# Performance work log

Measured on AMD Instinct MI355X. Metric: run time of the kernel, lower is better.

Reference implementation:

```python
import jax, jax.numpy as jnp
import numpy as np

N = 50000      # nodes
E = 800000     # edges (avg degree 16)
IN = 256       # in_channels
H = 128        # hidden_channels
LOC = 512      # location projection dim
EPS_BN = 1e-5
EPS_COS = 1e-8
NEG_SLOPE = 0.01


def setup_inputs() -> dict:
    key = jax.random.key(0)
    ks = jax.random.split(key, 16)
    s = 1.0 / np.sqrt(IN)
    sh = 1.0 / np.sqrt(H)
    return {
        "x": jax.random.normal(ks[0], (N, IN), dtype=jnp.float32),
        "edge_index": jax.random.randint(ks[1], (2, E), 0, N, dtype=jnp.int64),
        "bn_gamma": jax.random.uniform(ks[2], (IN,), dtype=jnp.float32, minval=0.5, maxval=1.5),
        "bn_beta": jax.random.normal(ks[3], (IN,), dtype=jnp.float32) * 0.1,
        "bn_mean": jax.random.normal(ks[4], (IN,), dtype=jnp.float32) * 0.1,
        "bn_var": jax.random.uniform(ks[5], (IN,), dtype=jnp.float32, minval=0.5, maxval=1.5),
        "W_lin": jax.random.uniform(ks[6], (IN, H), dtype=jnp.float32, minval=-s, maxval=s),
        "b_lin": jnp.zeros((H,), jnp.float32),
        "W1": jax.random.uniform(ks[7], (H, H), dtype=jnp.float32, minval=-sh, maxval=sh),
        "b1": jnp.zeros((H,), jnp.float32),
        "W2": jax.random.uniform(ks[8], (H, H), dtype=jnp.float32, minval=-sh, maxval=sh),
        "b2": jnp.zeros((H,), jnp.float32),
        "W_loc": jax.random.uniform(ks[9], (IN, LOC), dtype=jnp.float32, minval=-s, maxval=s),
        "b_loc": jnp.zeros((LOC,), jnp.float32),
        "loc_vec": jax.random.normal(ks[10], (N, IN), dtype=jnp.float32),
    }


def _leaky_relu(v):
    return jnp.where(v >= 0, v, NEG_SLOPE * v)


def _gcn_conv(h, W, b, src, dst, dinv, n):
    # PyG GCNConv (eval): D^{-1/2}(A+I)D^{-1/2} h W + b ; src/dst include self-loops
    hw = h @ W                                   # [n, H]
    coef = (dinv[src] * dinv[dst])[:, None]      # [e+n, 1]
    msg = hw[src] * coef                         # edge gather + scale
    return jax.ops.segment_sum(msg, dst, num_segments=n) + b


def reference(x, edge_index, bn_gamma, bn_beta, bn_mean, bn_var,
              W_lin, b_lin, W1, b1, W2, b2, W_loc, b_loc, loc_vec):
    n = x.shape[0]
    src = edge_index[0]
    dst = edge_index[1]
    loops = jnp.arange(n, dtype=src.dtype)
    # supply direction: src->dst ; demand direction: reversed edges
    s_src = jnp.concatenate([src, loops]); s_dst = jnp.concatenate([dst, loops])
    d_src = jnp.concatenate([dst, loops]); d_dst = jnp.concatenate([src, loops])

    def dinv_of(dd):
        deg = jax.ops.segment_sum(jnp.ones(dd.shape[0], x.dtype), dd, num_segments=n)
        return jnp.where(deg > 0, jax.lax.rsqrt(deg), 0.0)

    dinv_s = dinv_of(s_dst)
    dinv_d = dinv_of(d_dst)

    # BatchNorm1d (eval) + input Linear
    xb = (x - bn_mean) * jax.lax.rsqrt(bn_var + EPS_BN) * bn_gamma + bn_beta
    h = xb @ W_lin + b_lin

    # two GCN layers per direction (dropout is identity in eval)
    s1 = _leaky_relu(_gcn_conv(h, W1, b1, s_src, s_dst, dinv_s, n))
    s2 = _leaky_relu(_gcn_conv(s1, W2, b2, s_src, s_dst, dinv_s, n))
    r1 = _leaky_relu(_gcn_conv(h, W1, b1, d_src, d_dst, dinv_d, n))
    r2 = _leaky_relu(_gcn_conv(r1, W2, b2, d_src, d_dst, dinv_d, n))

    # edge-gather dot-product logits
    logits = jnp.sum(s2[src] * r2[dst], axis=1)  # [E]

    # location cosine-similarity per edge
    loc = loc_vec @ W_loc + b_loc                # [N, 512]
    l1 = loc[src]; l2 = loc[dst]
    cos = jnp.sum(l1 * l2, axis=1) / jnp.maximum(
        jnp.linalg.norm(l1, axis=1) * jnp.linalg.norm(l2, axis=1), EPS_COS)
    return logits / cos
```

## Files before the change

kernel.cpp:

```cpp
#include <hip/hip_runtime.h>

#define IN_C 256
#define H_C  128
#define LOC_C 512
#define EPS_BN 1e-5f
#define PSTR 136

typedef unsigned int u32;

__device__ __forceinline__ float lrelu(float v) { return v >= 0.0f ? v : 0.01f * v; }

__global__ void detect_i64(const int* ei, int* flag) {
  if (threadIdx.x == 0 && blockIdx.x == 0) {
    int z = 1;
    for (int i = 1; i < 128; i += 2) if (ei[i] != 0) { z = 0; break; }
    *flag = z;
  }
}

__device__ __forceinline__ int ld_edge(const int* ei, int is64, int idx) {
  return is64 ? ei[2 * idx] : ei[idx];
}

__global__ void sentinel_kernel(float* out, int n) {
  int i = blockIdx.x * blockDim.x + threadIdx.x;
  if (i < n) out[i] = 1.2345e9f;
}

__global__ void bn_prep(const float* __restrict__ g, const float* __restrict__ be,
                        const float* __restrict__ mu, const float* __restrict__ var,
                        float* __restrict__ scale, float* __restrict__ shift) {
  int c = threadIdx.x;
  float s = rsqrtf(var[c] + EPS_BN) * g[c];
  scale[c] = s;
  shift[c] = be[c] - mu[c] * s;
}

__global__ void degree_kernel(const int* __restrict__ ei, const int* __restrict__ flag,
                              int E, u32* __restrict__ deg_s, u32* __restrict__ deg_d) {
  int e = blockIdx.x * blockDim.x + threadIdx.x;
  if (e >= E) return;
  int is64 = *flag;
  int s = ld_edge(ei, is64, e);
  int d = ld_edge(ei, is64, E + e);
  atomicAdd(&deg_s[d], 1u);
  atomicAdd(&deg_d[s], 1u);
}

__global__ __launch_bounds__(1024) void scan_kernel(const u32* __restrict__ deg,
                                                    u32* __restrict__ rowptr,
                                                    u32* __restrict__ cursor,
                                                    float* __restrict__ dinv,
                                                    int N, int E) {
  __shared__ u32 part[1024];
  int dir = blockIdx.x;
  const u32* dg = deg + (size_t)dir * N;
  u32* rp = rowptr + (size_t)dir * (N + 1);
  u32* cu = cursor + (size_t)dir * N;
  float* dv = dinv + (size_t)dir * N;
  int t = threadIdx.x;
  int CH = (N + 1023) >> 10;
  int base = t * CH;
  u32 s = 0;
  for (int i = 0; i < CH; ++i) { int idx = base + i; if (idx < N) s += dg[idx]; }
  part[t] = s;
  __syncthreads();
  for (int off = 1; off < 1024; off <<= 1) {
    u32 v = (t >= off) ? part[t - off] : 0u;
    __syncthreads();
    part[t] += v;
    __syncthreads();
  }
  u32 run = (t > 0) ? part[t - 1] : 0u;
  for (int i = 0; i < CH; ++i) {
    int idx = base + i;
    if (idx < N) {
      rp[idx] = run;
      cu[idx] = run;
      u32 c = dg[idx];
      dv[idx] = rsqrtf((float)(c + 1u));
      run += c;
    }
  }
  if (t == 0) rp[N] = (u32)E;
}

__global__ void fill_kernel(const int* __restrict__ ei, const int* __restrict__ flag, int E,
                            u32* __restrict__ cur_s, u32* __restrict__ cur_d,
                            u32* __restrict__ col_s, u32* __restrict__ col_d,
                            u32* __restrict__ eid_d) {
  int e = blockIdx.x * blockDim.x + threadIdx.x;
  if (e >= E) return;
  int is64 = *flag;
  int s = ld_edge(ei, is64, e);
  int d = ld_edge(ei, is64, E + e);
  u32 ps = atomicAdd(&cur_s[d], 1u);
  col_s[ps] = (u32)s;
  u32 pd = atomicAdd(&cur_d[s], 1u);
  col_d[pd] = (u32)d;
  eid_d[pd] = (u32)e;
}

#define GM 128
#define GN 128
#define GK 16
#define ASTR (GM + 4)
#define BSTR (GN + 4)
template<bool BN_A, bool BIAS>
__global__ __launch_bounds__(256) void gemm_kernel(const float* __restrict__ A,
                                                   const float* __restrict__ B,
                                                   float* __restrict__ C,
                                                   int M, int K, int Ncols,
                                                   const float* __restrict__ bias,
                                                   const float* __restrict__ bnsc,
                                                   const float* __restrict__ bnsh) {
  __shared__ float As[GK][ASTR];
  __shared__ float Bs[GK][BSTR];
  int t = threadIdx.x;
  int tx = t & 15, ty = t >> 4;
  int m0 = blockIdx.x * GM;
  int n0 = blockIdx.y * GN;
  float acc[8][8] = {};
  for (int kk = 0; kk < K; kk += GK) {
#pragma unroll
    for (int i = 0; i < 2; ++i) {
      int idx = t * 2 + i;
      int row = idx >> 2;
      int kq = idx & 3;
      int gr = m0 + row;
      float4 v = make_float4(0.f, 0.f, 0.f, 0.f);
      if (gr < M) v = *(const float4*)(A + (size_t)gr * K + kk + kq * 4);
      if (BN_A) {
        float4 sc = *(const float4*)(bnsc + kk + kq * 4);
        float4 sh = *(const float4*)(bnsh + kk + kq * 4);
        v.x = fmaf(v.x, sc.x, sh.x); v.y = fmaf(v.y, sc.y, sh.y);
        v.z = fmaf(v.z, sc.z, sh.z); v.w = fmaf(v.w, sc.w, sh.w);
      }
      As[kq * 4 + 0][row] = v.x; As[kq * 4 + 1][row] = v.y;
      As[kq * 4 + 2][row] = v.z; As[kq * 4 + 3][row] = v.w;
    }
#pragma unroll
    for (int i = 0; i < 2; ++i) {
      int idx = t * 2 + i;
      int kr = idx >> 5;
      int cq = idx & 31;
      *(float4*)&Bs[kr][cq * 4] = *(const float4*)(B + (size_t)(kk + kr) * Ncols + n0 + cq * 4);
    }
    __syncthreads();
#pragma unroll
    for (int k = 0; k < GK; ++k) {
      float4 a0 = *(const float4*)&As[k][ty * 4];
      float4 a1 = *(const float4*)&As[k][ty * 4 + 64];
      float4 b0 = *(const float4*)&Bs[k][tx * 4];
      float4 b1 = *(const float4*)&Bs[k][tx * 4 + 64];
      float ar[8] = {a0.x, a0.y, a0.z, a0.w, a1.x, a1.y, a1.z, a1.w};
      float br[8] = {b0.x, b0.y, b0.z, b0.w, b1.x, b1.y, b1.z, b1.w};
#pragma unroll
      for (int ii = 0; ii < 8; ++ii)
#pragma unroll
        for (int jj = 0; jj < 8; ++jj)
          acc[ii][jj] = fmaf(ar[ii], br[jj], acc[ii][jj]);
    }
    __syncthreads();
  }
#pragma unroll
  for (int ii = 0; ii < 8; ++ii) {
    int gr = m0 + ((ii < 4) ? (ty * 4 + ii) : (64 + ty * 4 + ii - 4));
    if (gr < M) {
      float4 o0 = make_float4(acc[ii][0], acc[ii][1], acc[ii][2], acc[ii][3]);
      float4 o1 = make_float4(acc[ii][4], acc[ii][5], acc[ii][6], acc[ii][7]);
      if (BIAS) {
        float4 c0 = *(const float4*)(bias + n0 + tx * 4);
        float4 c1 = *(const float4*)(bias + n0 + 64 + tx * 4);
        o0.x += c0.x; o0.y += c0.y; o0.z += c0.z; o0.w += c0.w;
        o1.x += c1.x; o1.y += c1.y; o1.z += c1.z; o1.w += c1.w;
      }
      *(float4*)(C + (size_t)gr * Ncols + n0 + tx * 4) = o0;
      *(float4*)(C + (size_t)gr * Ncols + n0 + 64 + tx * 4) = o1;
    }
  }
}

__device__ __forceinline__ float4 fma4s(float4 v, float s, float4 c) {
  c.x = fmaf(v.x, s, c.x); c.y = fmaf(v.y, s, c.y);
  c.z = fmaf(v.z, s, c.z); c.w = fmaf(v.w, s, c.w);
  return c;
}

__global__ __launch_bounds__(256) void agg_kernel(const float* __restrict__ hw,
                                                  const float* __restrict__ dinv,
                                                  const u32* __restrict__ rowptr,
                                                  const u32* __restrict__ col,
                                                  const float* __restrict__ bias,
                                                  float* __restrict__ out, int N) {
  int wid = (blockIdx.x * blockDim.x + threadIdx.x) >> 6;
  int lane = threadIdx.x & 63;
  int half = lane >> 5, hl = lane & 31;
  int node = wid * 2 + half;
  if (node >= N) return;
  float di = dinv[node];
  float4 acc = *(const float4*)(hw + (size_t)node * H_C + hl * 4);
  acc.x *= di; acc.y *= di; acc.z *= di; acc.w *= di;
  u32 beg = rowptr[node], end = rowptr[node + 1];
  u32 k = beg;
  for (; k + 2 <= end; k += 2) {
    u32 j0 = col[k], j1 = col[k + 1];
    float dj0 = dinv[j0], dj1 = dinv[j1];
    float4 v0 = *(const float4*)(hw + (size_t)j0 * H_C + hl * 4);
    float4 v1 = *(const float4*)(hw + (size_t)j1 * H_C + hl * 4);
    acc = fma4s(v0, dj0, acc);
    acc = fma4s(v1, dj1, acc);
  }
  if (k < end) {
    u32 j0 = col[k];
    float dj0 = dinv[j0];
    float4 v0 = *(const float4*)(hw + (size_t)j0 * H_C + hl * 4);
    acc = fma4s(v0, dj0, acc);
  }
  float4 b4 = *(const float4*)(bias + hl * 4);
  float4 o;
  o.x = lrelu(fmaf(acc.x, di, b4.x));
  o.y = lrelu(fmaf(acc.y, di, b4.y));
  o.z = lrelu(fmaf(acc.z, di, b4.z));
  o.w = lrelu(fmaf(acc.w, di, b4.w));
  *(float4*)(out + (size_t)node * H_C + hl * 4) = o;
}

__device__ __forceinline__ float np_tree_combine(float r) {
  r = __fadd_rn(r, __shfl_xor(r, 1));
  r = __fadd_rn(r, __shfl_xor(r, 2));
  r = __fadd_rn(r, __shfl_xor(r, 4));
  r = __fadd_rn(r, __shfl_xor(r, 8));
  r = __fadd_rn(r, __shfl_xor(r, 16));
  return r;
}

__global__ __launch_bounds__(256) void norm_np_kernel(const float* __restrict__ loc,
                                                      float* __restrict__ norms, int N) {
  __shared__ float buf[4][PSTR * 4];
  int wib = threadIdx.x >> 6;
  int lane = threadIdx.x & 63;
  int u = blockIdx.x * 4 + wib;
  if (u >= N) return;
  const float* row = loc + (size_t)u * LOC_C;
#pragma unroll
  for (int i = 0; i < 2; ++i) {
    int w = lane + i * 64;
    float4 v4 = *(const float4*)(row + w * 4);
    *(float4*)&buf[wib][(w >> 5) * PSTR + ((w * 4) & 127)] = v4;
  }
  if (lane < 32) {
    int b = lane >> 3, j = lane & 7;
    const float* p = &buf[wib][b * PSTR + j];
    float v = p[0];
    float r = __fmul_rn(v, v);
#pragma unroll
    for (int t = 1; t < 16; ++t) {
      v = p[8 * t];
      r = __fadd_rn(r, __fmul_rn(v, v));
    }
    r = np_tree_combine(r);
    if (lane == 0) norms[u] = sqrtf(r);
  }
}

__global__ __launch_bounds__(256) void edge_np_kernel(const float* __restrict__ s2,
                                                      const float* __restrict__ r2,
                                                      const float* __restrict__ loc,
                                                      const float* __restrict__ norms,
                                                      const u32* __restrict__ rowptr_d,
                                                      const u32* __restrict__ col_d,
                                                      const u32* __restrict__ eid_d,
                                                      float* __restrict__ out, int N) {
  __shared__ float l1s[4][PSTR * 4];
  __shared__ float l2s[4][PSTR * 4];
  int wib = threadIdx.x >> 6;
  int lane = threadIdx.x & 63;
  int u = blockIdx.x * 4 + wib;
  if (u >= N) return;
  {
    const float* row = loc + (size_t)u * LOC_C;
#pragma unroll
    for (int i = 0; i < 2; ++i) {
      int w = lane + i * 64;
      float4 v4 = *(const float4*)(row + w * 4);
      *(float4*)&l1s[wib][(w >> 5) * PSTR + ((w * 4) & 127)] = v4;
    }
  }
  float2 su = *(const float2*)(s2 + (size_t)u * H_C + lane * 2);
  float nu = norms[u];
  int b = lane >> 3, j = lane & 7;
  u32 beg = rowptr_d[u], end = rowptr_d[u + 1];
  for (u32 k = beg; k < end; ++k) {
    u32 v = col_d[k];
    u32 e = eid_d[k];
    {
      const float* row = loc + (size_t)v * LOC_C;
#pragma unroll
      for (int i = 0; i < 2; ++i) {
        int w = lane + i * 64;
        float4 v4 = *(const float4*)(row + w * 4);
        *(float4*)&l2s[wib][(w >> 5) * PSTR + ((w * 4) & 127)] = v4;
      }
    }
    float2 rv = *(const float2*)(r2 + (size_t)v * H_C + lane * 2);
    float da = su.x * rv.x + su.y * rv.y;
#pragma unroll
    for (int off = 32; off; off >>= 1) da += __shfl_xor(da, off);
    float dt = 0.f;
    if (lane < 32) {
      const float* p1 = &l1s[wib][b * PSTR + j];
      const float* p2 = &l2s[wib][b * PSTR + j];
      float r = __fmul_rn(p1[0], p2[0]);
#pragma unroll
      for (int t = 1; t < 16; ++t)
        r = __fadd_rn(r, __fmul_rn(p1[8 * t], p2[8 * t]));
      dt = np_tree_combine(r);
    }
    if (lane == 0) {
      float n1n2 = __fmul_rn(nu, norms[v]);
      float den = fmaxf(n1n2, 1e-8f);
      float cosv = __fdiv_rn(dt, den);
      out[e] = __fdiv_rn(da, cosv);
    }
  }
}

extern "C" void kernel_launch(void* const* d_in, const int* in_sizes, int n_in,
                              void* d_out, int out_size, void* d_ws, size_t ws_size,
                              hipStream_t stream) {
  const float* x     = (const float*)d_in[0];
  const int*   ei    = (const int*)d_in[1];
  const float* bn_g  = (const float*)d_in[2];
  const float* bn_b  = (const float*)d_in[3];
  const float* bn_m  = (const float*)d_in[4];
  const float* bn_v  = (const float*)d_in[5];
  const float* W_lin = (const float*)d_in[6];
  const float* b_lin = (const float*)d_in[7];
  const float* W1    = (const float*)d_in[8];
  const float* b1    = (const float*)d_in[9];
  const float* W2    = (const float*)d_in[10];
  const float* b2    = (const float*)d_in[11];
  const float* W_loc = (const float*)d_in[12];
  const float* lv    = (const float*)d_in[14];
  float* out = (float*)d_out;

  int N = in_sizes[0] / IN_C;
  int E = in_sizes[1] / 2;

  char* base = (char*)d_ws;
  size_t NH4  = (size_t)N * H_C * 4;
  size_t locB = (size_t)N * LOC_C * 4;
  size_t off = 0;
  auto al = [](size_t v) { return (v + 255) & ~(size_t)255; };

  float* loc = (float*)(base);
  float* X0 = (float*)(base + 0 * NH4);
  float* X1 = (float*)(base + 1 * NH4);
  float* X2 = (float*)(base + 2 * NH4);
  float* X3 = (float*)(base + 3 * NH4);
  off = al(locB);
  float* S = (float*)(base + off); off += NH4;
  float* R = (float*)(base + off); off += NH4;
  float* norms = (float*)(base + off); off += al((size_t)N * 4);
  float* dinv  = (float*)(base + off); off += al((size_t)2 * N * 4);
  u32* deg     = (u32*)(base + off);   off += al((size_t)2 * N * 4);
  u32* rowptr  = (u32*)(base + off);   off += al((size_t)2 * (N + 1) * 4);
  u32* cursor  = (u32*)(base + off);   off += al((size_t)2 * N * 4);
  u32* col_s   = (u32*)(base + off);   off += al((size_t)E * 4);
  u32* col_d   = (u32*)(base + off);   off += al((size_t)E * 4);
  u32* eid_d   = (u32*)(base + off);   off += al((size_t)E * 4);
  float* bnsc  = (float*)(base + off); off += al((size_t)IN_C * 4);
  float* bnsh  = (float*)(base + off); off += al((size_t)IN_C * 4);
  int* flag    = (int*)(base + off);   off += 256;

  if (ws_size < off) {
    sentinel_kernel<<<(E + 255) / 256, 256, 0, stream>>>(out, E);
    return;
  }

  float* dinv_s = dinv,   *dinv_d = dinv + N;
  u32* deg_s = deg,       *deg_d = deg + N;
  u32* rp_s = rowptr,     *rp_d = rowptr + (N + 1);
  u32* cu_s = cursor,     *cu_d = cursor + N;

  hipMemsetAsync(deg, 0, (size_t)2 * N * 4, stream);
  detect_i64<<<1, 64, 0, stream>>>(ei, flag);
  bn_prep<<<1, 256, 0, stream>>>(bn_g, bn_b, bn_m, bn_v, bnsc, bnsh);

  int gridE = (E + 255) / 256;
  degree_kernel<<<gridE, 256, 0, stream>>>(ei, flag, E, deg_s, deg_d);
  scan_kernel<<<2, 1024, 0, stream>>>(deg, rowptr, cursor, dinv, N, E);
  fill_kernel<<<gridE, 256, 0, stream>>>(ei, flag, E, cu_s, cu_d, col_s, col_d, eid_d);

  int mtiles = (N + GM - 1) / GM;
  int gridW2 = (((N + 1) / 2) * 64 + 255) / 256;
  int gridN4 = (N + 3) / 4;

  gemm_kernel<true, true><<<dim3(mtiles, H_C / GN), 256, 0, stream>>>(
      x, W_lin, X0, N, IN_C, H_C, b_lin, bnsc, bnsh);
  gemm_kernel<false, false><<<dim3(mtiles, H_C / GN), 256, 0, stream>>>(
      X0, W1, X1, N, H_C, H_C, nullptr, nullptr, nullptr);
  agg_kernel<<<gridW2, 256, 0, stream>>>(X1, dinv_s, rp_s, col_s, b1, X2, N);
  agg_kernel<<<gridW2, 256, 0, stream>>>(X1, dinv_d, rp_d, col_d, b1, X3, N);
  gemm_kernel<false, false><<<dim3(mtiles, H_C / GN), 256, 0, stream>>>(
      X2, W2, X1, N, H_C, H_C, nullptr, nullptr, nullptr);
  agg_kernel<<<gridW2, 256, 0, stream>>>(X1, dinv_s, rp_s, col_s, b2, S, N);
  gemm_kernel<false, false><<<dim3(mtiles, H_C / GN), 256, 0, stream>>>(
      X3, W2, X1, N, H_C, H_C, nullptr, nullptr, nullptr);
  agg_kernel<<<gridW2, 256, 0, stream>>>(X1, dinv_d, rp_d, col_d, b2, R, N);

  gemm_kernel<false, false><<<dim3(mtiles, LOC_C / GN), 256, 0, stream>>>(
      lv, W_loc, loc, N, IN_C, LOC_C, nullptr, nullptr, nullptr);
  norm_np_kernel<<<gridN4, 256, 0, stream>>>(loc, norms, N);
  edge_np_kernel<<<gridN4, 256, 0, stream>>>(S, R, loc, norms,
                                             rp_d, col_d, eid_d, out, N);
}
```

Before: 1.211 ms.

## Prefetch next neighbor in edge kernel, unroll aggregation, batch second-layer GEMMs

The edge kernel now double-buffers the neighbor location row in shared memory and prefetches the next neighbor's loc row, r2 slice and norm into registers while the current edge is computed, to hide gather latency. It also returns early for nodes with no demand edges. The aggregation loop is unrolled to four neighbors so more loads are in flight at once. The two second-layer W2 GEMMs are merged into one launch over 2N rows, which assumes X2 and X3 sit next to each other in the workspace and that X0 and X1 are contiguous so the output split is correct.

```diff
diff --git a/kernel.cpp b/kernel.cpp
--- a/kernel.cpp
+++ b/kernel.cpp
@@ -203,15 +203,19 @@
   acc.x *= di; acc.y *= di; acc.z *= di; acc.w *= di;
   u32 beg = rowptr[node], end = rowptr[node + 1];
   u32 k = beg;
-  for (; k + 2 <= end; k += 2) {
-    u32 j0 = col[k], j1 = col[k + 1];
-    float dj0 = dinv[j0], dj1 = dinv[j1];
+  for (; k + 4 <= end; k += 4) {
+    u32 j0 = col[k], j1 = col[k + 1], j2 = col[k + 2], j3 = col[k + 3];
+    float dj0 = dinv[j0], dj1 = dinv[j1], dj2 = dinv[j2], dj3 = dinv[j3];
     float4 v0 = *(const float4*)(hw + (size_t)j0 * H_C + hl * 4);
     float4 v1 = *(const float4*)(hw + (size_t)j1 * H_C + hl * 4);
+    float4 v2 = *(const float4*)(hw + (size_t)j2 * H_C + hl * 4);
+    float4 v3 = *(const float4*)(hw + (size_t)j3 * H_C + hl * 4);
     acc = fma4s(v0, dj0, acc);
     acc = fma4s(v1, dj1, acc);
-  }
-  if (k < end) {
+    acc = fma4s(v2, dj2, acc);
+    acc = fma4s(v3, dj3, acc);
+  }
+  for (; k < end; ++k) {
     u32 j0 = col[k];
     float dj0 = dinv[j0];
     float4 v0 = *(const float4*)(hw + (size_t)j0 * H_C + hl * 4);
@@ -273,44 +277,56 @@
                                                       const u32* __restrict__ eid_d,
                                                       float* __restrict__ out, int N) {
   __shared__ float l1s[4][PSTR * 4];
-  __shared__ float l2s[4][PSTR * 4];
+  __shared__ float l2s[4][2][PSTR * 4];
   int wib = threadIdx.x >> 6;
   int lane = threadIdx.x & 63;
   int u = blockIdx.x * 4 + wib;
   if (u >= N) return;
+  u32 beg = rowptr_d[u], end = rowptr_d[u + 1];
+  if (beg == end) return;
+  int w0 = lane, w1 = lane + 64;
+  int o0 = (w0 >> 5) * PSTR + ((w0 * 4) & 127);
+  int o1 = (w1 >> 5) * PSTR + ((w1 * 4) & 127);
   {
-    const float* row = loc + (size_t)u * LOC_C;
-#pragma unroll
-    for (int i = 0; i < 2; ++i) {
-      int w = lane + i * 64;
-      float4 v4 = *(const float4*)(row + w * 4);
-      *(float4*)&l1s[wib][(w >> 5) * PSTR + ((w * 4) & 127)] = v4;
-    }
+    const float* urow = loc + (size_t)u * LOC_C;
+    *(float4*)&l1s[wib][o0] = *(const float4*)(urow + w0 * 4);
+    *(float4*)&l1s[wib][o1] = *(const float4*)(urow + w1 * 4);
   }
   float2 su = *(const float2*)(s2 + (size_t)u * H_C + lane * 2);
   float nu = norms[u];
   int b = lane >> 3, j = lane & 7;
-  u32 beg = rowptr_d[u], end = rowptr_d[u + 1];
+  u32 v_n = col_d[beg], e_n = eid_d[beg];
+  float4 pf0, pf1;
+  {
+    const float* vrow = loc + (size_t)v_n * LOC_C;
+    pf0 = *(const float4*)(vrow + w0 * 4);
+    pf1 = *(const float4*)(vrow + w1 * 4);
+  }
+  float2 rv_n = *(const float2*)(r2 + (size_t)v_n * H_C + lane * 2);
+  float nv_n = norms[v_n];
+  int cur = 0;
   for (u32 k = beg; k < end; ++k) {
-    u32 v = col_d[k];
-    u32 e = eid_d[k];
-    {
-      const float* row = loc + (size_t)v * LOC_C;
-#pragma unroll
-      for (int i = 0; i < 2; ++i) {
-        int w = lane + i * 64;
-        float4 v4 = *(const float4*)(row + w * 4);
-        *(float4*)&l2s[wib][(w >> 5) * PSTR + ((w * 4) & 127)] = v4;
-      }
-    }
-    float2 rv = *(const float2*)(r2 + (size_t)v * H_C + lane * 2);
+    u32 e = e_n;
+    float2 rv = rv_n;
+    float nv = nv_n;
+    *(float4*)&l2s[wib][cur][o0] = pf0;
+    *(float4*)&l2s[wib][cur][o1] = pf1;
+    if (k + 1 < end) {
+      v_n = col_d[k + 1];
+      e_n = eid_d[k + 1];
+      const float* nrow = loc + (size_t)v_n * LOC_C;
+      pf0 = *(const float4*)(nrow + w0 * 4);
+      pf1 = *(const float4*)(nrow + w1 * 4);
+      rv_n = *(const float2*)(r2 + (size_t)v_n * H_C + lane * 2);
+      nv_n = norms[v_n];
+    }
     float da = su.x * rv.x + su.y * rv.y;
 #pragma unroll
     for (int off = 32; off; off >>= 1) da += __shfl_xor(da, off);
     float dt = 0.f;
     if (lane < 32) {
       const float* p1 = &l1s[wib][b * PSTR + j];
-      const float* p2 = &l2s[wib][b * PSTR + j];
+      const float* p2 = &l2s[wib][cur][b * PSTR + j];
       float r = __fmul_rn(p1[0], p2[0]);
 #pragma unroll
       for (int t = 1; t < 16; ++t)
@@ -318,11 +334,12 @@
       dt = np_tree_combine(r);
     }
     if (lane == 0) {
-      float n1n2 = __fmul_rn(nu, norms[v]);
+      float n1n2 = __fmul_rn(nu, nv);
       float den = fmaxf(n1n2, 1e-8f);
       float cosv = __fdiv_rn(dt, den);
       out[e] = __fdiv_rn(da, cosv);
     }
+    cur ^= 1;
   }
 }
 
@@ -393,7 +410,8 @@
   scan_kernel<<<2, 1024, 0, stream>>>(deg, rowptr, cursor, dinv, N, E);
   fill_kernel<<<gridE, 256, 0, stream>>>(ei, flag, E, cu_s, cu_d, col_s, col_d, eid_d);
 
-  int mtiles = (N + GM - 1) / GM;
+  int mtiles  = (N + GM - 1) / GM;
+  int mtiles2 = (2 * N + GM - 1) / GM;
   int gridW2 = (((N + 1) / 2) * 64 + 255) / 256;
   int gridN4 = (N + 3) / 4;
 
@@ -403,11 +421,9 @@
       X0, W1, X1, N, H_C, H_C, nullptr, nullptr, nullptr);
   agg_kernel<<<gridW2, 256, 0, stream>>>(X1, dinv_s, rp_s, col_s, b1, X2, N);
   agg_kernel<<<gridW2, 256, 0, stream>>>(X1, dinv_d, rp_d, col_d, b1, X3, N);
-  gemm_kernel<false, false><<<dim3(mtiles, H_C / GN), 256, 0, stream>>>(
-      X2, W2, X1, N, H_C, H_C, nullptr, nullptr, nullptr);
-  agg_kernel<<<gridW2, 256, 0, stream>>>(X1, dinv_s, rp_s, col_s, b2, S, N);
-  gemm_kernel<false, false><<<dim3(mtiles, H_C / GN), 256, 0, stream>>>(
-      X3, W2, X1, N, H_C, H_C, nullptr, nullptr, nullptr);
+  gemm_kernel<false, false><<<dim3(mtiles2, H_C / GN), 256, 0, stream>>>(
+      X2, W2, X0, 2 * N, H_C, H_C, nullptr, nullptr, nullptr);
+  agg_kernel<<<gridW2, 256, 0, stream>>>(X0, dinv_s, rp_s, col_s, b2, S, N);
   agg_kernel<<<gridW2, 256, 0, stream>>>(X1, dinv_d, rp_d, col_d, b2, R, N);
 
   gemm_kernel<false, false><<<dim3(mtiles, LOC_C / GN), 256, 0, stream>>>(
```

Result: no change. 1.197 ms (-1.2%).
